# Kernel optimization log

Hardware: AMD Instinct MI355X
Metric: run time of the kernel (lower is better)

The kernel has to match this reference:

```python
import jax, jax.numpy as jnp
import numpy as np

B, L, D = 4, 4096, 1024


def setup_inputs() -> dict:
    key = jax.random.key(0)
    ks = jax.random.split(key, 10)
    x = jax.random.normal(ks[0], (B, L, D), dtype=jnp.float32)
    time_decay = jax.random.normal(ks[1], (D,), dtype=jnp.float32) * 0.1 - 5.0
    time_first = jax.random.normal(ks[2], (D,), dtype=jnp.float32) * 0.01
    time_mix_k = jnp.ones((D,), jnp.float32) * 0.5
    time_mix_v = jnp.ones((D,), jnp.float32) * 0.5
    time_mix_r = jnp.ones((D,), jnp.float32) * 0.5
    s = 1.0 / np.sqrt(D)
    Wk = jax.random.normal(ks[3], (D, D), dtype=jnp.float32) * s
    Wv = jax.random.normal(ks[4], (D, D), dtype=jnp.float32) * s
    Wr = jax.random.normal(ks[5], (D, D), dtype=jnp.float32) * s
    Wo = jax.random.normal(ks[6], (D, D), dtype=jnp.float32) * s
    return {"x": x, "time_decay": time_decay, "time_first": time_first,
            "time_mix_k": time_mix_k, "time_mix_v": time_mix_v, "time_mix_r": time_mix_r,
            "Wk": Wk, "Wv": Wv, "Wr": Wr, "Wo": Wo}


def _wkv_scan(k, v, w, u):
    # k, v: [B, L, D]; w, u: [D]. Sequential linear recurrence over L.
    decay = jnp.exp(w)  # per-channel decay factor e^{w}, w = -exp(time_decay) < 0
    Bb, Ll, Dd = k.shape

    def step(carry, kv_t):
        a, b = carry  # [B, D] numerator / denominator states
        k_t, v_t = kv_t
        ek_u = jnp.exp(u + k_t)
        wkv = (a + ek_u * v_t) / jnp.maximum(b + ek_u, 1e-6)
        ek = jnp.exp(k_t)
        return (decay * a + ek * v_t, decay * b + ek), wkv

    init = (jnp.zeros((Bb, Dd), k.dtype), jnp.zeros((Bb, Dd), k.dtype))
    _, out = jax.lax.scan(step, init, (jnp.swapaxes(k, 0, 1), jnp.swapaxes(v, 0, 1)))
    return jnp.swapaxes(out, 0, 1)  # [B, L, D]


def reference(x, time_decay, time_first, time_mix_k, time_mix_v, time_mix_r, Wk, Wv, Wr, Wo):
    Ll = x.shape[1]
    # token shift: x_prev[t] = x[t-1], zeros at t=0
    x_prev = jnp.pad(x, ((0, 0), (1, 0), (0, 0)))[:, :Ll]
    xk = x * time_mix_k + x_prev * (1.0 - time_mix_k)
    xv = x * time_mix_v + x_prev * (1.0 - time_mix_v)
    xr = x * time_mix_r + x_prev * (1.0 - time_mix_r)
    k = jnp.einsum('bld,ed->ble', xk, Wk)
    v = jnp.einsum('bld,ed->ble', xv, Wv)
    r = jax.nn.sigmoid(jnp.einsum('bld,ed->ble', xr, Wr))
    w = -jnp.exp(time_decay)
    wkv = _wkv_scan(k, v, w, time_first)
    return jnp.einsum('bld,ed->ble', r * wkv, Wo)
```

## Files before the change

### kernel.cpp

```cpp
#include <hip/hip_runtime.h>
#include <cstdint>
#include <cstddef>

typedef __bf16 bf16;
typedef __bf16 bf16x4 __attribute__((ext_vector_type(4)));
typedef __bf16 bf16x8 __attribute__((ext_vector_type(8)));
typedef float floatx4 __attribute__((ext_vector_type(4)));
typedef float floatx8 __attribute__((ext_vector_type(8)));
typedef unsigned int u32;

constexpr int Bb = 4, Ll = 4096, Dd = 1024;
constexpr int M  = Bb * Ll;
constexpr int NC = 64, CT = 64;

typedef const __attribute__((address_space(1))) u32 glb_u32;
typedef __attribute__((address_space(3))) u32 lds_u32;
__device__ __forceinline__ void gld16(const bf16* g, bf16* l) {
  __builtin_amdgcn_global_load_lds((glb_u32*)g, (lds_u32*)l, 16, 0, 0);
}
__device__ __forceinline__ void bar() {
  __builtin_amdgcn_s_barrier();
  asm volatile("" ::: "memory");
}

__global__ __launch_bounds__(256) void convw(
    const float* __restrict__ W, bf16* __restrict__ Wb)
{
  size_t base = ((size_t)blockIdx.x * 256 + threadIdx.x) * 8;
  floatx8 w = *(const floatx8*)(W + base);
  bf16x8 o;
  #pragma unroll
  for (int j = 0; j < 8; ++j) o[j] = (bf16)w[j];
  *(bf16x8*)(Wb + base) = o;
}

__global__ __launch_bounds__(256) void convw3(
    const float* __restrict__ Wa, const float* __restrict__ Wbp, const float* __restrict__ Wc,
    bf16* __restrict__ oa, bf16* __restrict__ ob, bf16* __restrict__ oc)
{
  const float* s = blockIdx.y == 0 ? Wa : (blockIdx.y == 1 ? Wbp : Wc);
  bf16*        d = blockIdx.y == 0 ? oa : (blockIdx.y == 1 ? ob  : oc);
  size_t base = ((size_t)blockIdx.x * 256 + threadIdx.x) * 8;
  floatx8 w = *(const floatx8*)(s + base);
  bf16x8 o;
  #pragma unroll
  for (int j = 0; j < 8; ++j) o[j] = (bf16)w[j];
  *(bf16x8*)(d + base) = o;
}

__global__ __launch_bounds__(256) void prep3(
    const float* __restrict__ x, const float* __restrict__ ma, const float* __restrict__ mb,
    const float* __restrict__ mc,
    bf16* __restrict__ oa, bf16* __restrict__ ob, bf16* __restrict__ oc)
{
  size_t base = ((size_t)blockIdx.x * 256 + threadIdx.x) * 8;
  int d = (int)(base & (size_t)(Dd - 1));
  int l = (int)((base / Dd) & (size_t)(Ll - 1));
  floatx8 xc = *(const floatx8*)(x + base);
  floatx8 xp = l ? *(const floatx8*)(x + base - Dd) : (floatx8)(0.0f);
  floatx8 a = *(const floatx8*)(ma + d);
  floatx8 b = *(const floatx8*)(mb + d);
  floatx8 c = *(const floatx8*)(mc + d);
  bf16x8 ra, rb, rc;
  #pragma unroll
  for (int j = 0; j < 8; ++j) {
    ra[j] = (bf16)(xc[j] * a[j] + xp[j] * (1.0f - a[j]));
    rb[j] = (bf16)(xc[j] * b[j] + xp[j] * (1.0f - b[j]));
    rc[j] = (bf16)(xc[j] * c[j] + xp[j] * (1.0f - c[j]));
  }
  *(bf16x8*)(oa + base) = ra;
  *(bf16x8*)(ob + base) = rb;
  *(bf16x8*)(oc + base) = rc;
}

template <int ACT>
__global__ __launch_bounds__(512, 2) void gemm8(
    const bf16* __restrict__ A, const bf16* __restrict__ W, void* __restrict__ Cout)
{
  __shared__ __align__(16) bf16 sm[65536];
  const int tid  = threadIdx.x;
  const int lane = tid & 63;
  const int w    = tid >> 6;
  const int wm   = (w >> 2) * 128;
  const int wn   = (w & 3) * 64;
  const int fr   = lane & 15;
  const int cu   = lane >> 4;
  const int key  = fr & 7;
  const int sw0  = ((cu)     ^ key) * 8;
  const int sw1  = ((4 | cu) ^ key) * 8;
  const int aro  = wm + fr;
  const int bro  = wn + fr;

  const int flat = (int)(blockIdx.y * 4 + blockIdx.x);
  const int nid  = (flat & 7) * 32 + (flat >> 3);
  const int m0   = (nid >> 2) * 256, n0 = (nid & 3) * 256;

  const int w0_ = tid, w1_ = tid + 512;
  const int lr0 = w0_ >> 3, sc0 = ((w0_ & 7) ^ (lr0 & 7)) * 8;
  const int lr1 = w1_ >> 3, sc1 = ((w1_ & 7) ^ (lr1 & 7)) * 8;
  const size_t rA0 = (size_t)(m0 + lr0) * Dd + sc0;
  const size_t rA1 = (size_t)(m0 + lr1) * Dd + sc1;
  const size_t rB0 = (size_t)(n0 + lr0) * Dd + sc0;
  const size_t rB1 = (size_t)(n0 + lr1) * Dd + sc1;
  const size_t HSTEP = (size_t)128 * Dd;

  floatx4 acc[8][4];
  #pragma unroll
  for (int i = 0; i < 8; ++i)
    #pragma unroll
    for (int j = 0; j < 4; ++j)
      acc[i][j] = (floatx4)(0.0f);

  {
    bf16* A0 = sm;
    bf16* B0 = sm + 16384;
    gld16(A + rA0,         A0 + (size_t)w0_ * 8);
    gld16(A + rA1,         A0 + (size_t)w1_ * 8);
    gld16(A + rA0 + HSTEP, A0 + 8192 + (size_t)w0_ * 8);
    gld16(A + rA1 + HSTEP, A0 + 8192 + (size_t)w1_ * 8);
    gld16(W + rB0,         B0 + (size_t)w0_ * 8);
    gld16(W + rB1,         B0 + (size_t)w1_ * 8);
    gld16(W + rB0 + HSTEP, B0 + 8192 + (size_t)w0_ * 8);
    gld16(W + rB1 + HSTEP, B0 + 8192 + (size_t)w1_ * 8);
    asm volatile("s_waitcnt vmcnt(0)" ::: "memory");
    bar();
  }

  bf16x8 a[8], bl[4], bh[4];
  #pragma unroll 2
  for (int t = 0; t < 16; ++t) {
    const int p = t & 1;
    bf16* Ap = sm + p * 32768;
    bf16* Bp = Ap + 16384;
    bf16* Aq = sm + (p ^ 1) * 32768;
    bf16* Bq = Aq + 16384;
    const size_t kn = (size_t)((t < 15 ? t + 1 : 15) * 64);

    #pragma unroll
    for (int i = 0; i < 4; ++i) {
      a[i * 2 + 0] = *(const bf16x8*)(Ap + (aro + i * 16) * 64 + sw0);
      a[i * 2 + 1] = *(const bf16x8*)(Ap + (aro + i * 16) * 64 + sw1);
    }
    #pragma unroll
    for (int j = 0; j < 2; ++j) {
      bl[j * 2 + 0] = *(const bf16x8*)(Bp + (bro + j * 16) * 64 + sw0);
      bl[j * 2 + 1] = *(const bf16x8*)(Bp + (bro + j * 16) * 64 + sw1);
    }
    gld16(A + rA0 + kn,         Aq + (size_t)w0_ * 8);
    gld16(A + rA1 + kn,         Aq + (size_t)w1_ * 8);
    gld16(A + rA0 + kn + HSTEP, Aq + 8192 + (size_t)w0_ * 8);
    gld16(A + rA1 + kn + HSTEP, Aq + 8192 + (size_t)w1_ * 8);
    bar();
    __builtin_amdgcn_s_setprio(1);
    #pragma unroll
    for (int ks = 0; ks < 2; ++ks)
      #pragma unroll
      for (int i = 0; i < 4; ++i)
        #pragma unroll
        for (int j = 0; j < 2; ++j)
          acc[i][j] = __builtin_amdgcn_mfma_f32_16x16x32_bf16(a[i * 2 + ks], bl[j * 2 + ks], acc[i][j], 0, 0, 0);
    __builtin_amdgcn_s_setprio(0);
    bar();

    #pragma unroll
    for (int j = 0; j < 2; ++j) {
      bh[j * 2 + 0] = *(const bf16x8*)(Bp + (bro + (j + 2) * 16) * 64 + sw0);
      bh[j * 2 + 1] = *(const bf16x8*)(Bp + (bro + (j + 2) * 16) * 64 + sw1);
    }
    gld16(W + rB0 + kn,         Bq + (size_t)w0_ * 8);
    gld16(W + rB1 + kn,         Bq + (size_t)w1_ * 8);
    gld16(W + rB0 + kn + HSTEP, Bq + 8192 + (size_t)w0_ * 8);
    gld16(W + rB1 + kn + HSTEP, Bq + 8192 + (size_t)w1_ * 8);
    bar();
    __builtin_amdgcn_s_setprio(1);
    #pragma unroll
    for (int ks = 0; ks < 2; ++ks)
      #pragma unroll
      for (int i = 0; i < 4; ++i)
        #pragma unroll
        for (int j = 0; j < 2; ++j)
          acc[i][j + 2] = __builtin_amdgcn_mfma_f32_16x16x32_bf16(a[i * 2 + ks], bh[j * 2 + ks], acc[i][j + 2], 0, 0, 0);
    __builtin_amdgcn_s_setprio(0);
    bar();

    #pragma unroll
    for (int i = 0; i < 4; ++i) {
      a[i * 2 + 0] = *(const bf16x8*)(Ap + (aro + (i + 4) * 16) * 64 + sw0);
      a[i * 2 + 1] = *(const bf16x8*)(Ap + (aro + (i + 4) * 16) * 64 + sw1);
    }
    bar();
    __builtin_amdgcn_s_setprio(1);
    #pragma unroll
    for (int ks = 0; ks < 2; ++ks)
      #pragma unroll
      for (int i = 0; i < 4; ++i)
        #pragma unroll
        for (int j = 0; j < 2; ++j)
          acc[i + 4][j + 2] = __builtin_amdgcn_mfma_f32_16x16x32_bf16(a[i * 2 + ks], bh[j * 2 + ks], acc[i + 4][j + 2], 0, 0, 0);
    __builtin_amdgcn_s_setprio(0);
    bar();

    asm volatile("s_waitcnt vmcnt(0)" ::: "memory");
    bar();
    __builtin_amdgcn_s_setprio(1);
    #pragma unroll
    for (int ks = 0; ks < 2; ++ks)
      #pragma unroll
      for (int i = 0; i < 4; ++i)
        #pragma unroll
        for (int j = 0; j < 2; ++j)
          acc[i + 4][j] = __builtin_amdgcn_mfma_f32_16x16x32_bf16(a[i * 2 + ks], bl[j * 2 + ks], acc[i + 4][j], 0, 0, 0);
    __builtin_amdgcn_s_setprio(0);
    bar();
  }
  asm volatile("s_waitcnt vmcnt(0)" ::: "memory");

  #pragma unroll
  for (int mi = 0; mi < 8; ++mi) {
    int rbase = m0 + wm + mi * 16 + (lane >> 4) * 4;
    #pragma unroll
    for (int j = 0; j < 4; ++j) {
      int col = n0 + wn + j * 16 + (lane & 15);
      #pragma unroll
      for (int r = 0; r < 4; ++r) {
        float v = acc[mi][j][r];
        size_t off = (size_t)(rbase + r) * Dd + col;
        if (ACT == 0)      ((float*)Cout)[off] = v;
        else if (ACT == 1) ((bf16*)Cout)[off]  = (bf16)(1.0f / (1.0f + __expf(-v)));
        else               ((bf16*)Cout)[off]  = (bf16)v;
      }
    }
  }
}

__global__ __launch_bounds__(256) void scan_partial(
    const bf16* __restrict__ k, const bf16* __restrict__ v,
    const float* __restrict__ td, float* __restrict__ Pa, float* __restrict__ Pb)
{
  const int pair = blockIdx.x;
  const int b = pair >> 6, c = pair & (NC - 1);
  const int d0 = threadIdx.x * 4;
  floatx4 tdv = *(const floatx4*)(td + d0);
  float decay[4], pa[4], pb[4];
  #pragma unroll
  for (int j = 0; j < 4; ++j) {
    decay[j] = __expf(-__expf(tdv[j]));
    pa[j] = 0.0f; pb[j] = 0.0f;
  }
  size_t base = ((size_t)(b * Ll + c * CT)) * Dd + d0;
  #pragma unroll 4
  for (int t = 0; t < CT; ++t) {
    size_t idx = base + (size_t)t * Dd;
    bf16x4 kk = *(const bf16x4*)(k + idx);
    bf16x4 vv = *(const bf16x4*)(v + idx);
    #pragma unroll
    for (int j = 0; j < 4; ++j) {
      float ek = __expf((float)kk[j]);
      pa[j] = decay[j] * pa[j] + ek * (float)vv[j];
      pb[j] = decay[j] * pb[j] + ek;
    }
  }
  size_t o = (size_t)pair * Dd + d0;
  floatx4 outa, outb;
  #pragma unroll
  for (int j = 0; j < 4; ++j) { outa[j] = pa[j]; outb[j] = pb[j]; }
  *(floatx4*)(Pa + o) = outa;
  *(floatx4*)(Pb + o) = outb;
}

__global__ __launch_bounds__(256) void scan_combine(
    const float* __restrict__ td, const float* __restrict__ Pa, const float* __restrict__ Pb,
    float* __restrict__ A0, float* __restrict__ B0)
{
  int d = blockIdx.x * 256 + threadIdx.x;
  int b = blockIdx.y;
  float dT = __expf(-__expf(td[d]) * (float)CT);
  float a = 0.0f, bb = 0.0f;
  for (int c = 0; c < NC; ++c) {
    size_t o = ((size_t)(b * NC + c)) * Dd + d;
    A0[o] = a; B0[o] = bb;
    a  = dT * a  + Pa[o];
    bb = dT * bb + Pb[o];
  }
}

__global__ __launch_bounds__(256) void scan_final(
    const bf16* __restrict__ k, bf16* __restrict__ vy, const bf16* __restrict__ r,
    const float* __restrict__ td, const float* __restrict__ tf,
    const float* __restrict__ A0, const float* __restrict__ B0)
{
  const int pair = blockIdx.x;
  const int b = pair >> 6, c = pair & (NC - 1);
  const int d0 = threadIdx.x * 4;
  floatx4 tdv = *(const floatx4*)(td + d0);
  floatx4 tfv = *(const floatx4*)(tf + d0);
  size_t o = (size_t)pair * Dd + d0;
  floatx4 av = *(const floatx4*)(A0 + o);
  floatx4 bv = *(const floatx4*)(B0 + o);
  float decay[4], u[4], a[4], bb[4];
  #pragma unroll
  for (int j = 0; j < 4; ++j) {
    decay[j] = __expf(-__expf(tdv[j]));
    u[j] = tfv[j]; a[j] = av[j]; bb[j] = bv[j];
  }
  size_t base = ((size_t)(b * Ll + c * CT)) * Dd + d0;
  #pragma unroll 2
  for (int t = 0; t < CT; ++t) {
    size_t idx = base + (size_t)t * Dd;
    bf16x4 kk = *(const bf16x4*)(k + idx);
    bf16x4 vv = *(const bf16x4*)(vy + idx);
    bf16x4 rr4 = *(const bf16x4*)(r + idx);
    bf16x4 y;
    #pragma unroll
    for (int j = 0; j < 4; ++j) {
      float kkj = (float)kk[j];
      float vvj = (float)vv[j];
      float eku = __expf(u[j] + kkj);
      float wkv = (a[j] + eku * vvj) / fmaxf(bb[j] + eku, 1e-6f);
      y[j] = (bf16)((float)rr4[j] * wkv);
      float ek = __expf(kkj);
      a[j]  = decay[j] * a[j]  + ek * vvj;
      bb[j] = decay[j] * bb[j] + ek;
    }
    *(bf16x4*)(vy + idx) = y;
  }
}

extern "C" void kernel_launch(void* const* d_in, const int* in_sizes, int n_in,
                              void* d_out, int out_size, void* d_ws, size_t ws_size,
                              hipStream_t stream)
{
  const float* x  = (const float*)d_in[0];
  const float* td = (const float*)d_in[1];
  const float* tf = (const float*)d_in[2];
  const float* mk = (const float*)d_in[3];
  const float* mv = (const float*)d_in[4];
  const float* mr = (const float*)d_in[5];
  const float* Wk = (const float*)d_in[6];
  const float* Wv = (const float*)d_in[7];
  const float* Wr = (const float*)d_in[8];
  const float* Wo = (const float*)d_in[9];
  float* out = (float*)d_out;

  char* ws = (char*)d_ws;
  const size_t S2 = (size_t)M * Dd * sizeof(bf16);
  const size_t SP = (size_t)Bb * NC * Dd;
  bf16* buf1 = (bf16*)(ws);
  bf16* buf2 = (bf16*)(ws + S2);
  bf16* buf3 = (bf16*)(ws + 2 * S2);
  float* Pa = (float*)(ws + 3 * S2);
  float* Pb = Pa + SP;
  float* A0 = Pb + SP;
  float* B0 = A0 + SP;

  char* ob  = (char*)d_out;
  bf16* rr  = (bf16*)d_out;
  bf16* Wkb = (bf16*)(ob + ((size_t)32 << 20));
  bf16* Wvb = (bf16*)(ob + ((size_t)34 << 20));
  bf16* Wrb = (bf16*)(ob + ((size_t)36 << 20));
  bf16* Wob = (bf16*)Pa;

  dim3 gp((unsigned)((size_t)M * Dd / (256 * 8)));
  dim3 gw((unsigned)((size_t)Dd * Dd / (256 * 8)));
  dim3 gg(Dd / 256, M / 256);

  convw3<<<dim3(gw.x, 3), 256, 0, stream>>>(Wk, Wv, Wr, Wkb, Wvb, Wrb);

  prep3<<<gp, 256, 0, stream>>>(x, mk, mv, mr, buf1, buf2, buf3);

  gemm8<1><<<gg, 512, 0, stream>>>(buf3, Wrb, rr);
  gemm8<2><<<gg, 512, 0, stream>>>(buf1, Wkb, buf3);
  gemm8<2><<<gg, 512, 0, stream>>>(buf2, Wvb, buf1);

  scan_partial<<<dim3(Bb * NC), 256, 0, stream>>>(buf3, buf1, td, Pa, Pb);
  scan_combine<<<dim3(Dd / 256, Bb), 256, 0, stream>>>(td, Pa, Pb, A0, B0);
  convw<<<gw, 256, 0, stream>>>(Wo, Wob);
  scan_final  <<<dim3(Bb * NC), 256, 0, stream>>>(buf3, buf1, rr, td, tf, A0, B0);

  gemm8<0><<<gg, 512, 0, stream>>>(buf1, Wob, out);
}
```

Baseline: 338.3 us.

## Replace GEMM with smaller-tile triple-buffered kernel using one barrier per K step

Replaces the 256x256x64 double-buffered GEMM with a 128x256x32 tile and a three-slot LDS ring. Each iteration waits on vmcnt(3) and crosses a single barrier, instead of the previous five or more barriers per K step. Smaller LDS use (72KB) and launch bounds of 4 are meant to raise occupancy, and the grid doubles to 512 blocks to fill the CUs better. In exchange, per-block arithmetic intensity falls, so more global and L2 traffic is needed for the same work.

```diff
diff --git a/kernel.cpp b/kernel.cpp
--- a/kernel.cpp
+++ b/kernel.cpp
@@ -74,149 +74,81 @@
 }
 
 template <int ACT>
-__global__ __launch_bounds__(512, 2) void gemm8(
+__global__ __launch_bounds__(512, 4) void gemmP(
     const bf16* __restrict__ A, const bf16* __restrict__ W, void* __restrict__ Cout)
 {
-  __shared__ __align__(16) bf16 sm[65536];
+  __shared__ __align__(16) bf16 sm[36864];
   const int tid  = threadIdx.x;
   const int lane = tid & 63;
   const int w    = tid >> 6;
-  const int wm   = (w >> 2) * 128;
+  const int wm   = (w >> 2) * 64;
   const int wn   = (w & 3) * 64;
   const int fr   = lane & 15;
   const int cu   = lane >> 4;
-  const int key  = fr & 7;
-  const int sw0  = ((cu)     ^ key) * 8;
-  const int sw1  = ((4 | cu) ^ key) * 8;
-  const int aro  = wm + fr;
-  const int bro  = wn + fr;
+  const int soff = ((cu ^ ((fr >> 1) & 3)) << 3);
 
   const int flat = (int)(blockIdx.y * 4 + blockIdx.x);
-  const int nid  = (flat & 7) * 32 + (flat >> 3);
-  const int m0   = (nid >> 2) * 256, n0 = (nid & 3) * 256;
-
-  const int w0_ = tid, w1_ = tid + 512;
-  const int lr0 = w0_ >> 3, sc0 = ((w0_ & 7) ^ (lr0 & 7)) * 8;
-  const int lr1 = w1_ >> 3, sc1 = ((w1_ & 7) ^ (lr1 & 7)) * 8;
-  const size_t rA0 = (size_t)(m0 + lr0) * Dd + sc0;
-  const size_t rA1 = (size_t)(m0 + lr1) * Dd + sc1;
-  const size_t rB0 = (size_t)(n0 + lr0) * Dd + sc0;
-  const size_t rB1 = (size_t)(n0 + lr1) * Dd + sc1;
-  const size_t HSTEP = (size_t)128 * Dd;
-
-  floatx4 acc[8][4];
-  #pragma unroll
-  for (int i = 0; i < 8; ++i)
+  const int nid  = (flat & 7) * 64 + (flat >> 3);
+  const int m0   = (nid >> 2) * 128, n0 = (nid & 3) * 256;
+
+  const int rA  = tid >> 2;
+  const int cA  = (((tid & 3) ^ ((rA >> 1) & 3)) << 3);
+  const int uB1 = tid + 512;
+  const int rB0 = tid >> 2, cB0 = cA;
+  const int rB1 = uB1 >> 2, cB1 = (((uB1 & 3) ^ ((rB1 >> 1) & 3)) << 3);
+  const bf16* gA  = A + (size_t)(m0 + rA)  * Dd + cA;
+  const bf16* gB0 = W + (size_t)(n0 + rB0) * Dd + cB0;
+  const bf16* gB1 = W + (size_t)(n0 + rB1) * Dd + cB1;
+
+  auto stage = [&](int slot, int t) {
+    const size_t kt = (size_t)(t > 31 ? 31 : t) * 32;
+    bf16* s = sm + slot * 12288;
+    gld16(gA  + kt, s + (size_t)tid * 8);
+    gld16(gB0 + kt, s + 4096 + (size_t)tid * 8);
+    gld16(gB1 + kt, s + 4096 + (size_t)uB1 * 8);
+  };
+
+  floatx4 acc[4][4];
+  #pragma unroll
+  for (int i = 0; i < 4; ++i)
     #pragma unroll
     for (int j = 0; j < 4; ++j)
       acc[i][j] = (floatx4)(0.0f);
 
-  {
-    bf16* A0 = sm;
-    bf16* B0 = sm + 16384;
-    gld16(A + rA0,         A0 + (size_t)w0_ * 8);
-    gld16(A + rA1,         A0 + (size_t)w1_ * 8);
-    gld16(A + rA0 + HSTEP, A0 + 8192 + (size_t)w0_ * 8);
-    gld16(A + rA1 + HSTEP, A0 + 8192 + (size_t)w1_ * 8);
-    gld16(W + rB0,         B0 + (size_t)w0_ * 8);
-    gld16(W + rB1,         B0 + (size_t)w1_ * 8);
-    gld16(W + rB0 + HSTEP, B0 + 8192 + (size_t)w0_ * 8);
-    gld16(W + rB1 + HSTEP, B0 + 8192 + (size_t)w1_ * 8);
-    asm volatile("s_waitcnt vmcnt(0)" ::: "memory");
+  stage(0, 0);
+  stage(1, 1);
+
+  bf16x8 a[4], b[4];
+  int scur = 0;
+  for (int t = 0; t < 32; ++t) {
+    asm volatile("s_waitcnt vmcnt(3)" ::: "memory");
     bar();
-  }
-
-  bf16x8 a[8], bl[4], bh[4];
-  #pragma unroll 2
-  for (int t = 0; t < 16; ++t) {
-    const int p = t & 1;
-    bf16* Ap = sm + p * 32768;
-    bf16* Bp = Ap + 16384;
-    bf16* Aq = sm + (p ^ 1) * 32768;
-    bf16* Bq = Aq + 16384;
-    const size_t kn = (size_t)((t < 15 ? t + 1 : 15) * 64);
-
-    #pragma unroll
-    for (int i = 0; i < 4; ++i) {
-      a[i * 2 + 0] = *(const bf16x8*)(Ap + (aro + i * 16) * 64 + sw0);
-      a[i * 2 + 1] = *(const bf16x8*)(Ap + (aro + i * 16) * 64 + sw1);
-    }
-    #pragma unroll
-    for (int j = 0; j < 2; ++j) {
-      bl[j * 2 + 0] = *(const bf16x8*)(Bp + (bro + j * 16) * 64 + sw0);
-      bl[j * 2 + 1] = *(const bf16x8*)(Bp + (bro + j * 16) * 64 + sw1);
-    }
-    gld16(A + rA0 + kn,         Aq + (size_t)w0_ * 8);
-    gld16(A + rA1 + kn,         Aq + (size_t)w1_ * 8);
-    gld16(A + rA0 + kn + HSTEP, Aq + 8192 + (size_t)w0_ * 8);
-    gld16(A + rA1 + kn + HSTEP, Aq + 8192 + (size_t)w1_ * 8);
-    bar();
+    int sstg = scur + 2; if (sstg >= 3) sstg -= 3;
+    stage(sstg, t + 2);
+
+    const bf16* sA = sm + scur * 12288;
+    const bf16* sB = sA + 4096;
+    #pragma unroll
+    for (int i = 0; i < 4; ++i)
+      a[i] = *(const bf16x8*)(sA + (wm + fr + i * 16) * 32 + soff);
+    #pragma unroll
+    for (int j = 0; j < 4; ++j)
+      b[j] = *(const bf16x8*)(sB + (wn + fr + j * 16) * 32 + soff);
+
     __builtin_amdgcn_s_setprio(1);
     #pragma unroll
-    for (int ks = 0; ks < 2; ++ks)
+    for (int i = 0; i < 4; ++i)
       #pragma unroll
-      for (int i = 0; i < 4; ++i)
-        #pragma unroll
-        for (int j = 0; j < 2; ++j)
-          acc[i][j] = __builtin_amdgcn_mfma_f32_16x16x32_bf16(a[i * 2 + ks], bl[j * 2 + ks], acc[i][j], 0, 0, 0);
+      for (int j = 0; j < 4; ++j)
+        acc[i][j] = __builtin_amdgcn_mfma_f32_16x16x32_bf16(a[i], b[j], acc[i][j], 0, 0, 0);
     __builtin_amdgcn_s_setprio(0);
-    bar();
-
-    #pragma unroll
-    for (int j = 0; j < 2; ++j) {
-      bh[j * 2 + 0] = *(const bf16x8*)(Bp + (bro + (j + 2) * 16) * 64 + sw0);
-      bh[j * 2 + 1] = *(const bf16x8*)(Bp + (bro + (j + 2) * 16) * 64 + sw1);
-    }
-    gld16(W + rB0 + kn,         Bq + (size_t)w0_ * 8);
-    gld16(W + rB1 + kn,         Bq + (size_t)w1_ * 8);
-    gld16(W + rB0 + kn + HSTEP, Bq + 8192 + (size_t)w0_ * 8);
-    gld16(W + rB1 + kn + HSTEP, Bq + 8192 + (size_t)w1_ * 8);
-    bar();
-    __builtin_amdgcn_s_setprio(1);
-    #pragma unroll
-    for (int ks = 0; ks < 2; ++ks)
-      #pragma unroll
-      for (int i = 0; i < 4; ++i)
-        #pragma unroll
-        for (int j = 0; j < 2; ++j)
-          acc[i][j + 2] = __builtin_amdgcn_mfma_f32_16x16x32_bf16(a[i * 2 + ks], bh[j * 2 + ks], acc[i][j + 2], 0, 0, 0);
-    __builtin_amdgcn_s_setprio(0);
-    bar();
-
-    #pragma unroll
-    for (int i = 0; i < 4; ++i) {
-      a[i * 2 + 0] = *(const bf16x8*)(Ap + (aro + (i + 4) * 16) * 64 + sw0);
-      a[i * 2 + 1] = *(const bf16x8*)(Ap + (aro + (i + 4) * 16) * 64 + sw1);
-    }
-    bar();
-    __builtin_amdgcn_s_setprio(1);
-    #pragma unroll
-    for (int ks = 0; ks < 2; ++ks)
-      #pragma unroll
-      for (int i = 0; i < 4; ++i)
-        #pragma unroll
-        for (int j = 0; j < 2; ++j)
-          acc[i + 4][j + 2] = __builtin_amdgcn_mfma_f32_16x16x32_bf16(a[i * 2 + ks], bh[j * 2 + ks], acc[i + 4][j + 2], 0, 0, 0);
-    __builtin_amdgcn_s_setprio(0);
-    bar();
-
-    asm volatile("s_waitcnt vmcnt(0)" ::: "memory");
-    bar();
-    __builtin_amdgcn_s_setprio(1);
-    #pragma unroll
-    for (int ks = 0; ks < 2; ++ks)
-      #pragma unroll
-      for (int i = 0; i < 4; ++i)
-        #pragma unroll
-        for (int j = 0; j < 2; ++j)
-          acc[i + 4][j] = __builtin_amdgcn_mfma_f32_16x16x32_bf16(a[i * 2 + ks], bl[j * 2 + ks], acc[i + 4][j], 0, 0, 0);
-    __builtin_amdgcn_s_setprio(0);
-    bar();
+
+    scur = (scur + 1 == 3) ? 0 : scur + 1;
   }
   asm volatile("s_waitcnt vmcnt(0)" ::: "memory");
 
   #pragma unroll
-  for (int mi = 0; mi < 8; ++mi) {
+  for (int mi = 0; mi < 4; ++mi) {
     int rbase = m0 + wm + mi * 16 + (lane >> 4) * 4;
     #pragma unroll
     for (int j = 0; j < 4; ++j) {
@@ -362,20 +294,20 @@
 
   dim3 gp((unsigned)((size_t)M * Dd / (256 * 8)));
   dim3 gw((unsigned)((size_t)Dd * Dd / (256 * 8)));
-  dim3 gg(Dd / 256, M / 256);
+  dim3 gg(Dd / 256, M / 128);
 
   convw3<<<dim3(gw.x, 3), 256, 0, stream>>>(Wk, Wv, Wr, Wkb, Wvb, Wrb);
 
   prep3<<<gp, 256, 0, stream>>>(x, mk, mv, mr, buf1, buf2, buf3);
 
-  gemm8<1><<<gg, 512, 0, stream>>>(buf3, Wrb, rr);
-  gemm8<2><<<gg, 512, 0, stream>>>(buf1, Wkb, buf3);
-  gemm8<2><<<gg, 512, 0, stream>>>(buf2, Wvb, buf1);
+  gemmP<1><<<gg, 512, 0, stream>>>(buf3, Wrb, rr);
+  gemmP<2><<<gg, 512, 0, stream>>>(buf1, Wkb, buf3);
+  gemmP<2><<<gg, 512, 0, stream>>>(buf2, Wvb, buf1);
 
   scan_partial<<<dim3(Bb * NC), 256, 0, stream>>>(buf3, buf1, td, Pa, Pb);
   scan_combine<<<dim3(Dd / 256, Bb), 256, 0, stream>>>(td, Pa, Pb, A0, B0);
   convw<<<gw, 256, 0, stream>>>(Wo, Wob);
   scan_final  <<<dim3(Bb * NC), 256, 0, stream>>>(buf3, buf1, rr, td, tf, A0, B0);
 
-  gemm8<0><<<gg, 512, 0, stream>>>(buf1, Wob, out);
-}
+  gemmP<0><<<gg, 512, 0, stream>>>(buf1, Wob, out);
+}
```

Result: slower. 348.3 us (+3.0%).
